# Performance work log

Measured on AMD Instinct MI355X. Metric: run time of the kernel, lower is better.

Reference implementation:

```python
import jax, jax.numpy as jnp
import numpy as np

B, S, D, H, HD = 4, 2048, 768, 12, 64


def setup_inputs() -> dict:
    key = jax.random.key(0)
    ks = jax.random.split(key, 9)
    s = 1.0 / np.sqrt(D)
    return {
        "hidden_state": jax.random.normal(ks[0], (B, S, D), jnp.float32),
        "Wq": jax.random.normal(ks[1], (H, D, HD), jnp.float32) * s,
        "bq": jax.random.normal(ks[2], (H, HD), jnp.float32) * 0.02,
        "Wk": jax.random.normal(ks[3], (H, D, HD), jnp.float32) * s,
        "bk": jax.random.normal(ks[4], (H, HD), jnp.float32) * 0.02,
        "Wv": jax.random.normal(ks[5], (H, D, HD), jnp.float32) * s,
        "bv": jax.random.normal(ks[6], (H, HD), jnp.float32) * 0.02,
        "Wo": jax.random.normal(ks[7], (D, D), jnp.float32) * s,
        "bo": jax.random.normal(ks[8], (D,), jnp.float32) * 0.02,
    }


def reference(hidden_state, Wq, bq, Wk, bk, Wv, bv, Wo, bo):
    # per-head projections, batched over heads: [B,H,S,HD]
    q = jnp.einsum("bsd,hde->bhse", hidden_state, Wq) + bq[None, :, None, :]
    k = jnp.einsum("bsd,hde->bhse", hidden_state, Wk) + bk[None, :, None, :]
    v = jnp.einsum("bsd,hde->bhse", hidden_state, Wv) + bv[None, :, None, :]
    scale = 1.0 / jnp.sqrt(jnp.asarray(HD, q.dtype))
    scores = jnp.einsum("bhse,bhte->bhst", q, k) * scale  # [B,H,S,S]
    attn = jax.nn.softmax(scores, axis=-1)
    out = jnp.einsum("bhst,bhte->bhse", attn, v)  # [B,H,S,HD]
    # concat heads in head order -> [B,S,D]
    out = out.transpose(0, 2, 1, 3).reshape(B, S, D)
    return out @ Wo.T + bo
```

## Files before the change

kernel.cpp:

```cpp
#include <hip/hip_runtime.h>
#include <hip/hip_bf16.h>

typedef unsigned short u16;
typedef __attribute__((ext_vector_type(8))) short short8;
typedef __attribute__((ext_vector_type(4))) float f32x4;

#define B_ 4
#define S_ 2048
#define D_ 768
#define H_ 12
#define HD_ 64

__device__ __forceinline__ u16 f2bf(float f) {
  union { float f; unsigned u; } c; c.f = f;
  unsigned u = c.u;
  unsigned lsb = (u >> 16) & 1u;
  u += 0x7fffu + lsb;
  return (u16)(u >> 16);
}

__device__ __forceinline__ unsigned cvt_pk(float lo, float hi) {
  unsigned r;
  asm("v_cvt_pk_bf16_f32 %0, %1, %2" : "=v"(r) : "v"(lo), "v"(hi));
  return r;
}

__global__ __launch_bounds__(256) void k_cvt_x(const float* __restrict__ x,
                                               u16* __restrict__ xb, int n4) {
  int i = blockIdx.x * 256 + threadIdx.x;
  if (i < n4) {
    float4 v = reinterpret_cast<const float4*>(x)[i];
    ushort4 o;
    unsigned c01 = cvt_pk(v.x, v.y), c23 = cvt_pk(v.z, v.w);
    o.x = (u16)c01; o.y = (u16)(c01 >> 16); o.z = (u16)c23; o.w = (u16)(c23 >> 16);
    reinterpret_cast<ushort4*>(xb)[i] = o;
  }
}

__global__ __launch_bounds__(256) void k_repack_qkv(const float* __restrict__ Wq,
                                                    const float* __restrict__ Wk,
                                                    const float* __restrict__ Wv,
                                                    u16* __restrict__ Wt) {
  const int h = blockIdx.x;
  const int d0 = blockIdx.y * 64;
  const int t = blockIdx.z;
  const float* W = (t == 0) ? Wq : (t == 1) ? Wk : Wv;
  const int tid = threadIdx.x;
  __shared__ __align__(16) u16 T[64][72];
#pragma unroll
  for (int i = 0; i < 16; i++) {
    int item = i * 256 + tid;
    int dl = item >> 6, e = item & 63;
    T[e][dl] = f2bf(W[h * (D_ * HD_) + (d0 + dl) * HD_ + e]);
  }
  __syncthreads();
#pragma unroll
  for (int i = 0; i < 4; i++) {
    int item = i * 256 + tid;
    int e = item >> 4, dl4 = (item & 15) * 4;
    ushort4 o = *reinterpret_cast<const ushort4*>(&T[e][dl4]);
    *reinterpret_cast<ushort4*>(&Wt[t * (D_ * D_) + (h * 64 + e) * D_ + d0 + dl4]) = o;
  }
}

__global__ __launch_bounds__(256) void k_gemm_qkv(const u16* __restrict__ Xb,
                                                  const u16* __restrict__ Wt,
                                                  const float* __restrict__ bq,
                                                  const float* __restrict__ bk,
                                                  u16* __restrict__ Qw,
                                                  u16* __restrict__ Kw) {
  const int t = blockIdx.z;
  const u16* Bmat = Wt + t * (D_ * D_);
  const float* bias = (t == 0) ? bq : bk;
  u16* Out = (t == 0) ? Qw : Kw;
  const float scale = (t == 0) ? 0.18033688f : 1.0f;
  const int m0 = blockIdx.x * 128, n0 = blockIdx.y * 128;
  __shared__ __align__(16) u16 Al[128][40];
  __shared__ __align__(16) u16 Bl[128][40];
  const int tid = threadIdx.x;
  const int lane = tid & 63, w = tid >> 6;
  const int wm = (w >> 1) * 64, wn = (w & 1) * 64;
  const int lg = lane >> 4, lr = lane & 15;
  const int sr0 = tid >> 2, sr1 = (tid + 256) >> 2;
  const int sc = (tid & 3) * 8;
  uint4 pa0, pa1, pb0, pb1;
  auto ld = [&](int k0) {
    pa0 = *reinterpret_cast<const uint4*>(&Xb[(m0 + sr0) * D_ + k0 + sc]);
    pa1 = *reinterpret_cast<const uint4*>(&Xb[(m0 + sr1) * D_ + k0 + sc]);
    pb0 = *reinterpret_cast<const uint4*>(&Bmat[(n0 + sr0) * D_ + k0 + sc]);
    pb1 = *reinterpret_cast<const uint4*>(&Bmat[(n0 + sr1) * D_ + k0 + sc]);
  };
  auto st_lds = [&]() {
    *reinterpret_cast<uint4*>(&Al[sr0][sc]) = pa0;
    *reinterpret_cast<uint4*>(&Al[sr1][sc]) = pa1;
    *reinterpret_cast<uint4*>(&Bl[sr0][sc]) = pb0;
    *reinterpret_cast<uint4*>(&Bl[sr1][sc]) = pb1;
  };
  f32x4 acc[4][4] = {};
  ld(0); st_lds();
  __syncthreads();
  for (int k0 = 0; k0 < D_; k0 += 32) {
    bool more = (k0 + 32) < D_;
    if (more) ld(k0 + 32);
    short8 af[4], bf[4];
#pragma unroll
    for (int i = 0; i < 4; i++)
      af[i] = *reinterpret_cast<const short8*>(&Al[wm + i * 16 + lr][lg * 8]);
#pragma unroll
    for (int i = 0; i < 4; i++)
      bf[i] = *reinterpret_cast<const short8*>(&Bl[wn + i * 16 + lr][lg * 8]);
#pragma unroll
    for (int mi = 0; mi < 4; mi++)
#pragma unroll
      for (int ni = 0; ni < 4; ni++)
        acc[mi][ni] = __builtin_amdgcn_mfma_f32_16x16x32_bf16(af[mi], bf[ni], acc[mi][ni], 0, 0, 0);
    if (more) {
      __syncthreads();
      st_lds();
      __syncthreads();
    }
  }
#pragma unroll
  for (int ni = 0; ni < 4; ni++) {
    int n = n0 + wn + ni * 16 + lr;
    float bns = bias[n] * scale;
    int h = n >> 6, e = n & 63;
#pragma unroll
    for (int mi = 0; mi < 4; mi++) {
      float v0 = fmaf(acc[mi][ni][0], scale, bns);
      float v1 = fmaf(acc[mi][ni][1], scale, bns);
      float v2 = fmaf(acc[mi][ni][2], scale, bns);
      float v3 = fmaf(acc[mi][ni][3], scale, bns);
      unsigned c01 = cvt_pk(v0, v1), c23 = cvt_pk(v2, v3);
      int m = m0 + wm + mi * 16 + lg * 4;
      int b = m >> 11, s = m & 2047;
      u16* base = &Out[((b * H_ + h) * S_ + s) * HD_ + e];
      base[0]       = (u16)c01;
      base[HD_]     = (u16)(c01 >> 16);
      base[2 * HD_] = (u16)c23;
      base[3 * HD_] = (u16)(c23 >> 16);
    }
  }
}

__global__ __launch_bounds__(256) void k_gemm_v(const u16* __restrict__ Xb,
                                                const u16* __restrict__ Wt,
                                                const float* __restrict__ bv,
                                                u16* __restrict__ VwT) {
  const u16* Bmat = Wt + 2 * (D_ * D_);
  const int m0 = blockIdx.x * 128, n0 = blockIdx.y * 128;
  __shared__ __align__(16) u16 Al[128][40];
  __shared__ __align__(16) u16 Bl[128][40];
  const int tid = threadIdx.x;
  const int lane = tid & 63, w = tid >> 6;
  const int wm = (w >> 1) * 64, wn = (w & 1) * 64;
  const int lg = lane >> 4, lr = lane & 15;
  const int sr0 = tid >> 2, sr1 = (tid + 256) >> 2;
  const int sc = (tid & 3) * 8;
  uint4 pa0, pa1, pb0, pb1;
  auto ld = [&](int k0) {
    pa0 = *reinterpret_cast<const uint4*>(&Xb[(m0 + sr0) * D_ + k0 + sc]);
    pa1 = *reinterpret_cast<const uint4*>(&Xb[(m0 + sr1) * D_ + k0 + sc]);
    pb0 = *reinterpret_cast<const uint4*>(&Bmat[(n0 + sr0) * D_ + k0 + sc]);
    pb1 = *reinterpret_cast<const uint4*>(&Bmat[(n0 + sr1) * D_ + k0 + sc]);
  };
  auto st_lds = [&]() {
    *reinterpret_cast<uint4*>(&Al[sr0][sc]) = pa0;
    *reinterpret_cast<uint4*>(&Al[sr1][sc]) = pa1;
    *reinterpret_cast<uint4*>(&Bl[sr0][sc]) = pb0;
    *reinterpret_cast<uint4*>(&Bl[sr1][sc]) = pb1;
  };
  f32x4 acc[4][4] = {};
  ld(0); st_lds();
  __syncthreads();
  for (int k0 = 0; k0 < D_; k0 += 32) {
    bool more = (k0 + 32) < D_;
    if (more) ld(k0 + 32);
    short8 af[4], bf[4];
#pragma unroll
    for (int i = 0; i < 4; i++)
      af[i] = *reinterpret_cast<const short8*>(&Al[wm + i * 16 + lr][lg * 8]);
#pragma unroll
    for (int i = 0; i < 4; i++)
      bf[i] = *reinterpret_cast<const short8*>(&Bl[wn + i * 16 + lr][lg * 8]);
#pragma unroll
    for (int ni = 0; ni < 4; ni++)
#pragma unroll
      for (int mi = 0; mi < 4; mi++)
        acc[ni][mi] = __builtin_amdgcn_mfma_f32_16x16x32_bf16(bf[ni], af[mi], acc[ni][mi], 0, 0, 0);
    if (more) {
      __syncthreads();
      st_lds();
      __syncthreads();
    }
  }
#pragma unroll
  for (int ni = 0; ni < 4; ni++) {
#pragma unroll
    for (int r = 0; r < 4; r++) {
      int n = n0 + wn + ni * 16 + lg * 4 + r;
      int h = n >> 6, e = n & 63;
      float bn = bv[n];
      float v0 = acc[ni][0][r] + bn, v1 = acc[ni][1][r] + bn;
      float v2 = acc[ni][2][r] + bn, v3 = acc[ni][3][r] + bn;
      unsigned c01 = cvt_pk(v0, v1), c23 = cvt_pk(v2, v3);
      int m = m0 + wm + lr;
      int b = m >> 11, s = m & 2047;
      u16* base = &VwT[((b * H_ + h) * HD_ + e) * S_ + s];
      base[0]  = (u16)c01;
      base[16] = (u16)(c01 >> 16);
      base[32] = (u16)c23;
      base[48] = (u16)(c23 >> 16);
    }
  }
}

__global__ __launch_bounds__(256) void k_attn(const u16* __restrict__ Qw,
                                              const u16* __restrict__ Kw,
                                              const u16* __restrict__ VwT,
                                              u16* __restrict__ An) {
  const int qb = blockIdx.x;
  const int bh = blockIdx.y;
  const int b = bh / H_, h = bh % H_;
  const int tid = threadIdx.x, lane = tid & 63, w = tid >> 6;
  const int lg = lane >> 4, lr = lane & 15;
  __shared__ __align__(16) u16 Kl[64][72];
  __shared__ __align__(16) u16 Vt[64][72];
  __shared__ __align__(16) u16 Pb[4][32][72];
  const u16* Qp = Qw + (bh * S_ + qb * 128 + w * 32) * HD_;
  const u16* Kp = Kw + bh * S_ * HD_;
  const u16* VTp = VwT + bh * HD_ * S_;
  const int srow0 = tid >> 3, srow1 = (tid + 256) >> 3;
  const int sch = (tid & 7) * 8;
  short8 qf[2][2];
#pragma unroll
  for (int qif = 0; qif < 2; qif++)
#pragma unroll
    for (int es = 0; es < 2; es++)
      qf[qif][es] = *reinterpret_cast<const short8*>(&Qp[(qif * 16 + lr) * HD_ + es * 32 + lg * 8]);
  f32x4 acc[2][4] = {};
  float mcol[2] = {-INFINITY, -INFINITY};
  float lcol[2] = {0.f, 0.f};

  {
    uint4 k0a = *reinterpret_cast<const uint4*>(&Kp[srow0 * HD_ + sch]);
    uint4 k0b = *reinterpret_cast<const uint4*>(&Kp[srow1 * HD_ + sch]);
    uint4 v0a = *reinterpret_cast<const uint4*>(&VTp[srow0 * S_ + sch]);
    uint4 v0b = *reinterpret_cast<const uint4*>(&VTp[srow1 * S_ + sch]);
    *reinterpret_cast<uint4*>(&Kl[srow0][sch]) = k0a;
    *reinterpret_cast<uint4*>(&Kl[srow1][sch]) = k0b;
    *reinterpret_cast<uint4*>(&Vt[srow0][sch]) = v0a;
    *reinterpret_cast<uint4*>(&Vt[srow1][sch]) = v0b;
  }
  __syncthreads();

  for (int t0 = 0; t0 < S_; t0 += 64) {
    const int tn = t0 + 64;
    uint4 kna, knb, vna, vnb;
    if (tn < S_) {
      kna = *reinterpret_cast<const uint4*>(&Kp[(tn + srow0) * HD_ + sch]);
      knb = *reinterpret_cast<const uint4*>(&Kp[(tn + srow1) * HD_ + sch]);
      vna = *reinterpret_cast<const uint4*>(&VTp[srow0 * S_ + tn + sch]);
      vnb = *reinterpret_cast<const uint4*>(&VTp[srow1 * S_ + tn + sch]);
    }
    f32x4 st[4][2] = {};
#pragma unroll
    for (int es = 0; es < 2; es++) {
      short8 kf[4];
#pragma unroll
      for (int kjf = 0; kjf < 4; kjf++)
        kf[kjf] = *reinterpret_cast<const short8*>(&Kl[kjf * 16 + lr][es * 32 + lg * 8]);
      __builtin_amdgcn_s_setprio(1);
#pragma unroll
      for (int kjf = 0; kjf < 4; kjf++)
#pragma unroll
        for (int qif = 0; qif < 2; qif++)
          st[kjf][qif] = __builtin_amdgcn_mfma_f32_16x16x32_bf16(kf[kjf], qf[qif][es], st[kjf][qif], 0, 0, 0);
      __builtin_amdgcn_s_setprio(0);
    }
#pragma unroll
    for (int qif = 0; qif < 2; qif++) {
      float tmax = st[0][qif][0];
#pragma unroll
      for (int kjf = 0; kjf < 4; kjf++)
#pragma unroll
        for (int r = 0; r < 4; r++) tmax = fmaxf(tmax, st[kjf][qif][r]);
      tmax = fmaxf(tmax, __shfl_xor(tmax, 16));
      tmax = fmaxf(tmax, __shfl_xor(tmax, 32));
      if (__any(tmax > mcol[qif] + 10.0f)) {
        float mnew = fmaxf(mcol[qif], tmax);
        float csc = exp2f(mcol[qif] - mnew);
        mcol[qif] = mnew;
        lcol[qif] *= csc;
#pragma unroll
        for (int r = 0; r < 4; r++) {
          float f = __shfl(csc, lg * 4 + r);
#pragma unroll
          for (int ef = 0; ef < 4; ef++) acc[qif][ef][r] *= f;
        }
      }
      float m = mcol[qif];
      float tsum = 0.f;
#pragma unroll
      for (int kjf = 0; kjf < 4; kjf++) {
        float p0 = exp2f(st[kjf][qif][0] - m);
        float p1 = exp2f(st[kjf][qif][1] - m);
        float p2 = exp2f(st[kjf][qif][2] - m);
        float p3 = exp2f(st[kjf][qif][3] - m);
        tsum += (p0 + p1) + (p2 + p3);
        uint2 pv;
        pv.x = cvt_pk(p0, p1);
        pv.y = cvt_pk(p2, p3);
        *reinterpret_cast<uint2*>(&Pb[w][qif * 16 + lr][kjf * 16 + lg * 4]) = pv;
      }
      tsum += __shfl_xor(tsum, 16);
      tsum += __shfl_xor(tsum, 32);
      lcol[qif] += tsum;
    }
#pragma unroll
    for (int ks = 0; ks < 2; ks++) {
      short8 pa[2];
#pragma unroll
      for (int qif = 0; qif < 2; qif++)
        pa[qif] = *reinterpret_cast<const short8*>(&Pb[w][qif * 16 + lr][ks * 32 + lg * 8]);
      __builtin_amdgcn_s_setprio(1);
#pragma unroll
      for (int ef = 0; ef < 4; ef++) {
        short8 vf = *reinterpret_cast<const short8*>(&Vt[ef * 16 + lr][ks * 32 + lg * 8]);
#pragma unroll
        for (int qif = 0; qif < 2; qif++)
          acc[qif][ef] = __builtin_amdgcn_mfma_f32_16x16x32_bf16(pa[qif], vf, acc[qif][ef], 0, 0, 0);
      }
      __builtin_amdgcn_s_setprio(0);
    }
    __syncthreads();
    if (tn < S_) {
      *reinterpret_cast<uint4*>(&Kl[srow0][sch]) = kna;
      *reinterpret_cast<uint4*>(&Kl[srow1][sch]) = knb;
      *reinterpret_cast<uint4*>(&Vt[srow0][sch]) = vna;
      *reinterpret_cast<uint4*>(&Vt[srow1][sch]) = vnb;
    }
    __syncthreads();
  }
  int qbase = qb * 128 + w * 32;
#pragma unroll
  for (int qif = 0; qif < 2; qif++) {
#pragma unroll
    for (int r = 0; r < 4; r++) {
      float lv = __shfl(lcol[qif], lg * 4 + r);
      float linv = 1.0f / lv;
      int s = qbase + qif * 16 + lg * 4 + r;
      u16* op = &An[(b * S_ + s) * D_ + h * HD_];
      float a0 = acc[qif][0][r] * linv, a1 = acc[qif][1][r] * linv;
      float a2 = acc[qif][2][r] * linv, a3 = acc[qif][3][r] * linv;
      unsigned c01 = cvt_pk(a0, a1), c23 = cvt_pk(a2, a3);
      op[0 * 16 + lr] = (u16)c01;
      op[1 * 16 + lr] = (u16)(c01 >> 16);
      op[2 * 16 + lr] = (u16)c23;
      op[3 * 16 + lr] = (u16)(c23 >> 16);
    }
  }
}

__global__ __launch_bounds__(256) void k_gemm_out(const u16* __restrict__ An,
                                                  const u16* __restrict__ Wob,
                                                  const float* __restrict__ bo,
                                                  float* __restrict__ out) {
  const int m0 = blockIdx.x * 128, n0 = blockIdx.y * 128;
  __shared__ __align__(16) u16 Al[128][40];
  __shared__ __align__(16) u16 Bl[128][40];
  const int tid = threadIdx.x;
  const int lane = tid & 63, w = tid >> 6;
  const int wm = (w >> 1) * 64, wn = (w & 1) * 64;
  const int lg = lane >> 4, lr = lane & 15;
  const int sr0 = tid >> 2, sr1 = (tid + 256) >> 2;
  const int sc = (tid & 3) * 8;
  uint4 pa0, pa1, pb0, pb1;
  auto ld = [&](int k0) {
    pa0 = *reinterpret_cast<const uint4*>(&An[(m0 + sr0) * D_ + k0 + sc]);
    pa1 = *reinterpret_cast<const uint4*>(&An[(m0 + sr1) * D_ + k0 + sc]);
    pb0 = *reinterpret_cast<const uint4*>(&Wob[(n0 + sr0) * D_ + k0 + sc]);
    pb1 = *reinterpret_cast<const uint4*>(&Wob[(n0 + sr1) * D_ + k0 + sc]);
  };
  auto st_lds = [&]() {
    *reinterpret_cast<uint4*>(&Al[sr0][sc]) = pa0;
    *reinterpret_cast<uint4*>(&Al[sr1][sc]) = pa1;
    *reinterpret_cast<uint4*>(&Bl[sr0][sc]) = pb0;
    *reinterpret_cast<uint4*>(&Bl[sr1][sc]) = pb1;
  };
  f32x4 acc[4][4] = {};
  ld(0); st_lds();
  __syncthreads();
  for (int k0 = 0; k0 < D_; k0 += 32) {
    bool more = (k0 + 32) < D_;
    if (more) ld(k0 + 32);
    short8 af[4], bf[4];
#pragma unroll
    for (int i = 0; i < 4; i++)
      af[i] = *reinterpret_cast<const short8*>(&Al[wm + i * 16 + lr][lg * 8]);
#pragma unroll
    for (int i = 0; i < 4; i++)
      bf[i] = *reinterpret_cast<const short8*>(&Bl[wn + i * 16 + lr][lg * 8]);
#pragma unroll
    for (int mi = 0; mi < 4; mi++)
#pragma unroll
      for (int ni = 0; ni < 4; ni++)
        acc[mi][ni] = __builtin_amdgcn_mfma_f32_16x16x32_bf16(af[mi], bf[ni], acc[mi][ni], 0, 0, 0);
    if (more) {
      __syncthreads();
      st_lds();
      __syncthreads();
    }
  }
#pragma unroll
  for (int ni = 0; ni < 4; ni++) {
    int n = n0 + wn + ni * 16 + lr;
    float bn = bo[n];
#pragma unroll
    for (int mi = 0; mi < 4; mi++) {
#pragma unroll
      for (int r = 0; r < 4; r++) {
        int m = m0 + wm + mi * 16 + lg * 4 + r;
        out[m * D_ + n] = acc[mi][ni][r] + bn;
      }
    }
  }
}

extern "C" void kernel_launch(void* const* d_in, const int* in_sizes, int n_in,
                              void* d_out, int out_size, void* d_ws, size_t ws_size,
                              hipStream_t stream) {
  const float* X  = (const float*)d_in[0];
  const float* Wq = (const float*)d_in[1];
  const float* bq = (const float*)d_in[2];
  const float* Wk = (const float*)d_in[3];
  const float* bk = (const float*)d_in[4];
  const float* Wv = (const float*)d_in[5];
  const float* bv = (const float*)d_in[6];
  const float* Wo = (const float*)d_in[7];
  const float* bo = (const float*)d_in[8];
  float* out = (float*)d_out;

  char* ws = (char*)d_ws;
  u16* Xb  = (u16*)(ws + 0);
  u16* Wt  = (u16*)(ws + 12582912);
  u16* Wob = (u16*)(ws + 16121856);
  u16* Qw  = (u16*)(ws + 17301504);
  u16* Kw  = (u16*)(ws + 29884416);
  u16* VwT = (u16*)(ws + 42467328);
  u16* An  = (u16*)(ws + 55050240);

  const int nx4 = (B_ * S_ * D_) / 4;
  const int nw4 = (D_ * D_) / 4;
  k_cvt_x<<<dim3(nx4 / 256), dim3(256), 0, stream>>>(X, Xb, nx4);
  k_cvt_x<<<dim3(nw4 / 256), dim3(256), 0, stream>>>(Wo, Wob, nw4);
  k_repack_qkv<<<dim3(12, 12, 3), dim3(256), 0, stream>>>(Wq, Wk, Wv, Wt);
  k_gemm_qkv<<<dim3(64, 6, 2), dim3(256), 0, stream>>>(Xb, Wt, bq, bk, Qw, Kw);
  k_gemm_v<<<dim3(64, 6), dim3(256), 0, stream>>>(Xb, Wt, bv, VwT);
  k_attn<<<dim3(16, 48), dim3(256), 0, stream>>>(Qw, Kw, VwT, An);
  k_gemm_out<<<dim3(64, 6), dim3(256), 0, stream>>>(An, Wob, bo, out);
}
```

Measured before the change: 297.0 us.

## Merge Q/K/V projection GEMMs and use 8 waves of 16 queries in attention

The separate V projection kernel is folded into the QK projection kernel as a third grid slice, so one launch covers all three projections and blocks from all slices can be co-scheduled. The attention kernel now runs 512 threads per block, with each wave handling 16 queries instead of 32. Each K/V tile loaded into shared memory is therefore shared by twice as many waves, and per-wave register pressure drops. The cost is half as many MFMAs per wave between barriers and more waves per block syncing, which could reduce MFMA efficiency.

```diff
diff --git a/kernel.cpp b/kernel.cpp
--- a/kernel.cpp
+++ b/kernel.cpp
@@ -63,16 +63,17 @@
   }
 }
 
-__global__ __launch_bounds__(256) void k_gemm_qkv(const u16* __restrict__ Xb,
-                                                  const u16* __restrict__ Wt,
-                                                  const float* __restrict__ bq,
-                                                  const float* __restrict__ bk,
-                                                  u16* __restrict__ Qw,
-                                                  u16* __restrict__ Kw) {
+__global__ __launch_bounds__(256) void k_gemm_proj(const u16* __restrict__ Xb,
+                                                   const u16* __restrict__ Wt,
+                                                   const float* __restrict__ bq,
+                                                   const float* __restrict__ bk,
+                                                   const float* __restrict__ bv,
+                                                   u16* __restrict__ Qw,
+                                                   u16* __restrict__ Kw,
+                                                   u16* __restrict__ VwT) {
   const int t = blockIdx.z;
   const u16* Bmat = Wt + t * (D_ * D_);
-  const float* bias = (t == 0) ? bq : bk;
-  u16* Out = (t == 0) ? Qw : Kw;
+  const float* bias = (t == 0) ? bq : (t == 1) ? bk : bv;
   const float scale = (t == 0) ? 0.18033688f : 1.0f;
   const int m0 = blockIdx.x * 128, n0 = blockIdx.y * 128;
   __shared__ __align__(16) u16 Al[128][40];
@@ -109,113 +110,72 @@
 #pragma unroll
     for (int i = 0; i < 4; i++)
       bf[i] = *reinterpret_cast<const short8*>(&Bl[wn + i * 16 + lr][lg * 8]);
-#pragma unroll
-    for (int mi = 0; mi < 4; mi++)
+    if (t < 2) {
+#pragma unroll
+      for (int mi = 0; mi < 4; mi++)
+#pragma unroll
+        for (int ni = 0; ni < 4; ni++)
+          acc[mi][ni] = __builtin_amdgcn_mfma_f32_16x16x32_bf16(af[mi], bf[ni], acc[mi][ni], 0, 0, 0);
+    } else {
 #pragma unroll
       for (int ni = 0; ni < 4; ni++)
-        acc[mi][ni] = __builtin_amdgcn_mfma_f32_16x16x32_bf16(af[mi], bf[ni], acc[mi][ni], 0, 0, 0);
+#pragma unroll
+        for (int mi = 0; mi < 4; mi++)
+          acc[ni][mi] = __builtin_amdgcn_mfma_f32_16x16x32_bf16(bf[ni], af[mi], acc[ni][mi], 0, 0, 0);
+    }
     if (more) {
       __syncthreads();
       st_lds();
       __syncthreads();
     }
   }
-#pragma unroll
-  for (int ni = 0; ni < 4; ni++) {
-    int n = n0 + wn + ni * 16 + lr;
-    float bns = bias[n] * scale;
-    int h = n >> 6, e = n & 63;
-#pragma unroll
-    for (int mi = 0; mi < 4; mi++) {
-      float v0 = fmaf(acc[mi][ni][0], scale, bns);
-      float v1 = fmaf(acc[mi][ni][1], scale, bns);
-      float v2 = fmaf(acc[mi][ni][2], scale, bns);
-      float v3 = fmaf(acc[mi][ni][3], scale, bns);
-      unsigned c01 = cvt_pk(v0, v1), c23 = cvt_pk(v2, v3);
-      int m = m0 + wm + mi * 16 + lg * 4;
-      int b = m >> 11, s = m & 2047;
-      u16* base = &Out[((b * H_ + h) * S_ + s) * HD_ + e];
-      base[0]       = (u16)c01;
-      base[HD_]     = (u16)(c01 >> 16);
-      base[2 * HD_] = (u16)c23;
-      base[3 * HD_] = (u16)(c23 >> 16);
-    }
-  }
-}
-
-__global__ __launch_bounds__(256) void k_gemm_v(const u16* __restrict__ Xb,
-                                                const u16* __restrict__ Wt,
-                                                const float* __restrict__ bv,
-                                                u16* __restrict__ VwT) {
-  const u16* Bmat = Wt + 2 * (D_ * D_);
-  const int m0 = blockIdx.x * 128, n0 = blockIdx.y * 128;
-  __shared__ __align__(16) u16 Al[128][40];
-  __shared__ __align__(16) u16 Bl[128][40];
-  const int tid = threadIdx.x;
-  const int lane = tid & 63, w = tid >> 6;
-  const int wm = (w >> 1) * 64, wn = (w & 1) * 64;
-  const int lg = lane >> 4, lr = lane & 15;
-  const int sr0 = tid >> 2, sr1 = (tid + 256) >> 2;
-  const int sc = (tid & 3) * 8;
-  uint4 pa0, pa1, pb0, pb1;
-  auto ld = [&](int k0) {
-    pa0 = *reinterpret_cast<const uint4*>(&Xb[(m0 + sr0) * D_ + k0 + sc]);
-    pa1 = *reinterpret_cast<const uint4*>(&Xb[(m0 + sr1) * D_ + k0 + sc]);
-    pb0 = *reinterpret_cast<const uint4*>(&Bmat[(n0 + sr0) * D_ + k0 + sc]);
-    pb1 = *reinterpret_cast<const uint4*>(&Bmat[(n0 + sr1) * D_ + k0 + sc]);
-  };
-  auto st_lds = [&]() {
-    *reinterpret_cast<uint4*>(&Al[sr0][sc]) = pa0;
-    *reinterpret_cast<uint4*>(&Al[sr1][sc]) = pa1;
-    *reinterpret_cast<uint4*>(&Bl[sr0][sc]) = pb0;
-    *reinterpret_cast<uint4*>(&Bl[sr1][sc]) = pb1;
-  };
-  f32x4 acc[4][4] = {};
-  ld(0); st_lds();
-  __syncthreads();
-  for (int k0 = 0; k0 < D_; k0 += 32) {
-    bool more = (k0 + 32) < D_;
-    if (more) ld(k0 + 32);
-    short8 af[4], bf[4];
-#pragma unroll
-    for (int i = 0; i < 4; i++)
-      af[i] = *reinterpret_cast<const short8*>(&Al[wm + i * 16 + lr][lg * 8]);
-#pragma unroll
-    for (int i = 0; i < 4; i++)
-      bf[i] = *reinterpret_cast<const short8*>(&Bl[wn + i * 16 + lr][lg * 8]);
-#pragma unroll
-    for (int ni = 0; ni < 4; ni++)
-#pragma unroll
-      for (int mi = 0; mi < 4; mi++)
-        acc[ni][mi] = __builtin_amdgcn_mfma_f32_16x16x32_bf16(bf[ni], af[mi], acc[ni][mi], 0, 0, 0);
-    if (more) {
-      __syncthreads();
-      st_lds();
-      __syncthreads();
-    }
-  }
-#pragma unroll
-  for (int ni = 0; ni < 4; ni++) {
-#pragma unroll
-    for (int r = 0; r < 4; r++) {
-      int n = n0 + wn + ni * 16 + lg * 4 + r;
+  if (t < 2) {
+    u16* Out = (t == 0) ? Qw : Kw;
+#pragma unroll
+    for (int ni = 0; ni < 4; ni++) {
+      int n = n0 + wn + ni * 16 + lr;
+      float bns = bias[n] * scale;
       int h = n >> 6, e = n & 63;
-      float bn = bv[n];
-      float v0 = acc[ni][0][r] + bn, v1 = acc[ni][1][r] + bn;
-      float v2 = acc[ni][2][r] + bn, v3 = acc[ni][3][r] + bn;
-      unsigned c01 = cvt_pk(v0, v1), c23 = cvt_pk(v2, v3);
-      int m = m0 + wm + lr;
-      int b = m >> 11, s = m & 2047;
-      u16* base = &VwT[((b * H_ + h) * HD_ + e) * S_ + s];
-      base[0]  = (u16)c01;
-      base[16] = (u16)(c01 >> 16);
-      base[32] = (u16)c23;
-      base[48] = (u16)(c23 >> 16);
-    }
-  }
-}
-
-__global__ __launch_bounds__(256) void k_attn(const u16* __restrict__ Qw,
+#pragma unroll
+      for (int mi = 0; mi < 4; mi++) {
+        float v0 = fmaf(acc[mi][ni][0], scale, bns);
+        float v1 = fmaf(acc[mi][ni][1], scale, bns);
+        float v2 = fmaf(acc[mi][ni][2], scale, bns);
+        float v3 = fmaf(acc[mi][ni][3], scale, bns);
+        unsigned c01 = cvt_pk(v0, v1), c23 = cvt_pk(v2, v3);
+        int m = m0 + wm + mi * 16 + lg * 4;
+        int b = m >> 11, s = m & 2047;
+        u16* base = &Out[((b * H_ + h) * S_ + s) * HD_ + e];
+        base[0]       = (u16)c01;
+        base[HD_]     = (u16)(c01 >> 16);
+        base[2 * HD_] = (u16)c23;
+        base[3 * HD_] = (u16)(c23 >> 16);
+      }
+    }
+  } else {
+#pragma unroll
+    for (int ni = 0; ni < 4; ni++) {
+#pragma unroll
+      for (int r = 0; r < 4; r++) {
+        int n = n0 + wn + ni * 16 + lg * 4 + r;
+        int h = n >> 6, e = n & 63;
+        float bn = bias[n];
+        float v0 = acc[ni][0][r] + bn, v1 = acc[ni][1][r] + bn;
+        float v2 = acc[ni][2][r] + bn, v3 = acc[ni][3][r] + bn;
+        unsigned c01 = cvt_pk(v0, v1), c23 = cvt_pk(v2, v3);
+        int m = m0 + wm + lr;
+        int b = m >> 11, s = m & 2047;
+        u16* base = &VwT[((b * H_ + h) * HD_ + e) * S_ + s];
+        base[0]  = (u16)c01;
+        base[16] = (u16)(c01 >> 16);
+        base[32] = (u16)c23;
+        base[48] = (u16)(c23 >> 16);
+      }
+    }
+  }
+}
+
+__global__ __launch_bounds__(512) void k_attn(const u16* __restrict__ Qw,
                                               const u16* __restrict__ Kw,
                                               const u16* __restrict__ VwT,
                                               u16* __restrict__ An) {
@@ -226,44 +186,36 @@
   const int lg = lane >> 4, lr = lane & 15;
   __shared__ __align__(16) u16 Kl[64][72];
   __shared__ __align__(16) u16 Vt[64][72];
-  __shared__ __align__(16) u16 Pb[4][32][72];
-  const u16* Qp = Qw + (bh * S_ + qb * 128 + w * 32) * HD_;
+  __shared__ __align__(16) u16 Pb[8][16][72];
+  const u16* Qp = Qw + (bh * S_ + qb * 128 + w * 16) * HD_;
   const u16* Kp = Kw + bh * S_ * HD_;
   const u16* VTp = VwT + bh * HD_ * S_;
-  const int srow0 = tid >> 3, srow1 = (tid + 256) >> 3;
+  const int srow = tid >> 3;
   const int sch = (tid & 7) * 8;
-  short8 qf[2][2];
-#pragma unroll
-  for (int qif = 0; qif < 2; qif++)
-#pragma unroll
-    for (int es = 0; es < 2; es++)
-      qf[qif][es] = *reinterpret_cast<const short8*>(&Qp[(qif * 16 + lr) * HD_ + es * 32 + lg * 8]);
-  f32x4 acc[2][4] = {};
-  float mcol[2] = {-INFINITY, -INFINITY};
-  float lcol[2] = {0.f, 0.f};
+  short8 qf[2];
+#pragma unroll
+  for (int es = 0; es < 2; es++)
+    qf[es] = *reinterpret_cast<const short8*>(&Qp[lr * HD_ + es * 32 + lg * 8]);
+  f32x4 acc[4] = {};
+  float mcol = -INFINITY;
+  float lcol = 0.f;
 
   {
-    uint4 k0a = *reinterpret_cast<const uint4*>(&Kp[srow0 * HD_ + sch]);
-    uint4 k0b = *reinterpret_cast<const uint4*>(&Kp[srow1 * HD_ + sch]);
-    uint4 v0a = *reinterpret_cast<const uint4*>(&VTp[srow0 * S_ + sch]);
-    uint4 v0b = *reinterpret_cast<const uint4*>(&VTp[srow1 * S_ + sch]);
-    *reinterpret_cast<uint4*>(&Kl[srow0][sch]) = k0a;
-    *reinterpret_cast<uint4*>(&Kl[srow1][sch]) = k0b;
-    *reinterpret_cast<uint4*>(&Vt[srow0][sch]) = v0a;
-    *reinterpret_cast<uint4*>(&Vt[srow1][sch]) = v0b;
+    uint4 k0 = *reinterpret_cast<const uint4*>(&Kp[srow * HD_ + sch]);
+    uint4 v0 = *reinterpret_cast<const uint4*>(&VTp[srow * S_ + sch]);
+    *reinterpret_cast<uint4*>(&Kl[srow][sch]) = k0;
+    *reinterpret_cast<uint4*>(&Vt[srow][sch]) = v0;
   }
   __syncthreads();
 
   for (int t0 = 0; t0 < S_; t0 += 64) {
     const int tn = t0 + 64;
-    uint4 kna, knb, vna, vnb;
+    uint4 kn, vn;
     if (tn < S_) {
-      kna = *reinterpret_cast<const uint4*>(&Kp[(tn + srow0) * HD_ + sch]);
-      knb = *reinterpret_cast<const uint4*>(&Kp[(tn + srow1) * HD_ + sch]);
-      vna = *reinterpret_cast<const uint4*>(&VTp[srow0 * S_ + tn + sch]);
-      vnb = *reinterpret_cast<const uint4*>(&VTp[srow1 * S_ + tn + sch]);
-    }
-    f32x4 st[4][2] = {};
+      kn = *reinterpret_cast<const uint4*>(&Kp[(tn + srow) * HD_ + sch]);
+      vn = *reinterpret_cast<const uint4*>(&VTp[srow * S_ + tn + sch]);
+    }
+    f32x4 st[4] = {};
 #pragma unroll
     for (int es = 0; es < 2; es++) {
       short8 kf[4];
@@ -273,92 +225,79 @@
       __builtin_amdgcn_s_setprio(1);
 #pragma unroll
       for (int kjf = 0; kjf < 4; kjf++)
-#pragma unroll
-        for (int qif = 0; qif < 2; qif++)
-          st[kjf][qif] = __builtin_amdgcn_mfma_f32_16x16x32_bf16(kf[kjf], qf[qif][es], st[kjf][qif], 0, 0, 0);
+        st[kjf] = __builtin_amdgcn_mfma_f32_16x16x32_bf16(kf[kjf], qf[es], st[kjf], 0, 0, 0);
       __builtin_amdgcn_s_setprio(0);
     }
-#pragma unroll
-    for (int qif = 0; qif < 2; qif++) {
-      float tmax = st[0][qif][0];
+    {
+      float tmax = st[0][0];
 #pragma unroll
       for (int kjf = 0; kjf < 4; kjf++)
 #pragma unroll
-        for (int r = 0; r < 4; r++) tmax = fmaxf(tmax, st[kjf][qif][r]);
+        for (int r = 0; r < 4; r++) tmax = fmaxf(tmax, st[kjf][r]);
       tmax = fmaxf(tmax, __shfl_xor(tmax, 16));
       tmax = fmaxf(tmax, __shfl_xor(tmax, 32));
-      if (__any(tmax > mcol[qif] + 10.0f)) {
-        float mnew = fmaxf(mcol[qif], tmax);
-        float csc = exp2f(mcol[qif] - mnew);
-        mcol[qif] = mnew;
-        lcol[qif] *= csc;
+      if (__any(tmax > mcol + 10.0f)) {
+        float mnew = fmaxf(mcol, tmax);
+        float csc = exp2f(mcol - mnew);
+        mcol = mnew;
+        lcol *= csc;
 #pragma unroll
         for (int r = 0; r < 4; r++) {
           float f = __shfl(csc, lg * 4 + r);
 #pragma unroll
-          for (int ef = 0; ef < 4; ef++) acc[qif][ef][r] *= f;
+          for (int ef = 0; ef < 4; ef++) acc[ef][r] *= f;
         }
       }
-      float m = mcol[qif];
+      float m = mcol;
       float tsum = 0.f;
 #pragma unroll
       for (int kjf = 0; kjf < 4; kjf++) {
-        float p0 = exp2f(st[kjf][qif][0] - m);
-        float p1 = exp2f(st[kjf][qif][1] - m);
-        float p2 = exp2f(st[kjf][qif][2] - m);
-        float p3 = exp2f(st[kjf][qif][3] - m);
+        float p0 = exp2f(st[kjf][0] - m);
+        float p1 = exp2f(st[kjf][1] - m);
+        float p2 = exp2f(st[kjf][2] - m);
+        float p3 = exp2f(st[kjf][3] - m);
         tsum += (p0 + p1) + (p2 + p3);
         uint2 pv;
         pv.x = cvt_pk(p0, p1);
         pv.y = cvt_pk(p2, p3);
-        *reinterpret_cast<uint2*>(&Pb[w][qif * 16 + lr][kjf * 16 + lg * 4]) = pv;
+        *reinterpret_cast<uint2*>(&Pb[w][lr][kjf * 16 + lg * 4]) = pv;
       }
       tsum += __shfl_xor(tsum, 16);
       tsum += __shfl_xor(tsum, 32);
-      lcol[qif] += tsum;
+      lcol += tsum;
     }
 #pragma unroll
     for (int ks = 0; ks < 2; ks++) {
-      short8 pa[2];
-#pragma unroll
-      for (int qif = 0; qif < 2; qif++)
-        pa[qif] = *reinterpret_cast<const short8*>(&Pb[w][qif * 16 + lr][ks * 32 + lg * 8]);
+      short8 pa = *reinterpret_cast<const short8*>(&Pb[w][lr][ks * 32 + lg * 8]);
       __builtin_amdgcn_s_setprio(1);
 #pragma unroll
       for (int ef = 0; ef < 4; ef++) {
         short8 vf = *reinterpret_cast<const short8*>(&Vt[ef * 16 + lr][ks * 32 + lg * 8]);
-#pragma unroll
-        for (int qif = 0; qif < 2; qif++)
-          acc[qif][ef] = __builtin_amdgcn_mfma_f32_16x16x32_bf16(pa[qif], vf, acc[qif][ef], 0, 0, 0);
+        acc[ef] = __builtin_amdgcn_mfma_f32_16x16x32_bf16(pa, vf, acc[ef], 0, 0, 0);
       }
       __builtin_amdgcn_s_setprio(0);
     }
     __syncthreads();
     if (tn < S_) {
-      *reinterpret_cast<uint4*>(&Kl[srow0][sch]) = kna;
-      *reinterpret_cast<uint4*>(&Kl[srow1][sch]) = knb;
-      *reinterpret_cast<uint4*>(&Vt[srow0][sch]) = vna;
-      *reinterpret_cast<uint4*>(&Vt[srow1][sch]) = vnb;
+      *reinterpret_cast<uint4*>(&Kl[srow][sch]) = kn;
+      *reinterpret_cast<uint4*>(&Vt[srow][sch]) = vn;
     }
     __syncthreads();
   }
-  int qbase = qb * 128 + w * 32;
-#pragma unroll
-  for (int qif = 0; qif < 2; qif++) {
-#pragma unroll
-    for (int r = 0; r < 4; r++) {
-      float lv = __shfl(lcol[qif], lg * 4 + r);
-      float linv = 1.0f / lv;
-      int s = qbase + qif * 16 + lg * 4 + r;
-      u16* op = &An[(b * S_ + s) * D_ + h * HD_];
-      float a0 = acc[qif][0][r] * linv, a1 = acc[qif][1][r] * linv;
-      float a2 = acc[qif][2][r] * linv, a3 = acc[qif][3][r] * linv;
-      unsigned c01 = cvt_pk(a0, a1), c23 = cvt_pk(a2, a3);
-      op[0 * 16 + lr] = (u16)c01;
-      op[1 * 16 + lr] = (u16)(c01 >> 16);
-      op[2 * 16 + lr] = (u16)c23;
-      op[3 * 16 + lr] = (u16)(c23 >> 16);
-    }
+  int qbase = qb * 128 + w * 16;
+#pragma unroll
+  for (int r = 0; r < 4; r++) {
+    float lv = __shfl(lcol, lg * 4 + r);
+    float linv = 1.0f / lv;
+    int s = qbase + lg * 4 + r;
+    u16* op = &An[(b * S_ + s) * D_ + h * HD_];
+    float a0 = acc[0][r] * linv, a1 = acc[1][r] * linv;
+    float a2 = acc[2][r] * linv, a3 = acc[3][r] * linv;
+    unsigned c01 = cvt_pk(a0, a1), c23 = cvt_pk(a2, a3);
+    op[0 * 16 + lr] = (u16)c01;
+    op[1 * 16 + lr] = (u16)(c01 >> 16);
+    op[2 * 16 + lr] = (u16)c23;
+    op[3 * 16 + lr] = (u16)(c23 >> 16);
   }
 }
 
@@ -455,8 +394,7 @@
   k_cvt_x<<<dim3(nx4 / 256), dim3(256), 0, stream>>>(X, Xb, nx4);
   k_cvt_x<<<dim3(nw4 / 256), dim3(256), 0, stream>>>(Wo, Wob, nw4);
   k_repack_qkv<<<dim3(12, 12, 3), dim3(256), 0, stream>>>(Wq, Wk, Wv, Wt);
-  k_gemm_qkv<<<dim3(64, 6, 2), dim3(256), 0, stream>>>(Xb, Wt, bq, bk, Qw, Kw);
-  k_gemm_v<<<dim3(64, 6), dim3(256), 0, stream>>>(Xb, Wt, bv, VwT);
-  k_attn<<<dim3(16, 48), dim3(256), 0, stream>>>(Qw, Kw, VwT, An);
+  k_gemm_proj<<<dim3(64, 6, 3), dim3(256), 0, stream>>>(Xb, Wt, bq, bk, bv, Qw, Kw, VwT);
+  k_attn<<<dim3(16, 48), dim3(512), 0, stream>>>(Qw, Kw, VwT, An);
   k_gemm_out<<<dim3(64, 6), dim3(256), 0, stream>>>(An, Wob, bo, out);
 }
```

Measured after the change: 284.5 us. -4.2%, faster.
